# Kernel optimization log

Measured on AMD Instinct MI355X. Metric: run time of the kernel, lower is better.

The kernel has to match this reference:

```python
import jax, jax.numpy as jnp
import numpy as np

C = 256  # input_channels == output_channels (residual add requires it)
EPS = 1e-5


def conv1d(x, w, b):
    # x: [B, Cin, L], w: [Cout, Cin, K], 'same' padding for K=3,p=1
    y = jax.lax.conv_general_dilated(x, w, window_strides=(1,), padding=[(1, 1)],
                                     dimension_numbers=('NCH', 'OIH', 'NCH'))
    return y + b[None, :, None]


def batchnorm(x, gamma, beta):
    # training-mode BN over (batch, length) per channel, biased variance
    m = jnp.mean(x, axis=(0, 2), keepdims=True)
    v = jnp.var(x, axis=(0, 2), keepdims=True)
    return (x - m) * jax.lax.rsqrt(v + EPS) * gamma[None, :, None] + beta[None, :, None]


def cross_attn(q_in, kv_in, res, qw, qb, kw, kb, vw, vb, ow, ob, g, be):
    q = conv1d(q_in, qw, qb)   # [B, C, L]
    k = conv1d(kv_in, kw, kb)  # [B, C, L]
    v = conv1d(kv_in, vw, vb)  # [B, C, L]
    scores = jnp.einsum('bcl,bcm->blm', q, k) / jnp.sqrt(jnp.float32(C))
    probs = jax.nn.softmax(scores, axis=-1)          # [B, L, L]
    ctx = jnp.einsum('blm,bcm->bcl', probs, v)       # [B, C, L]
    return batchnorm(conv1d(ctx, ow, ob), g, be) + res


def setup_inputs() -> dict:
    key = jax.random.key(0)
    ks = jax.random.split(key, 24)
    B, L = 16, 1024
    d = {
        'image': jax.random.normal(ks[0], (B, C, L), jnp.float32),
        'clinical': jax.random.normal(ks[1], (B, 1, L), jnp.float32),
    }
    def w(k, shape):
        return jax.random.normal(k, shape, jnp.float32) * 0.05
    # branch a: cli_to_img (query from image, key/value from clinical)
    d['a_qw'] = w(ks[2], (C, C, 3)); d['a_qb'] = w(ks[3], (C,))
    d['a_kw'] = w(ks[4], (C, 1, 3)); d['a_kb'] = w(ks[5], (C,))
    d['a_vw'] = w(ks[6], (C, 1, 3)); d['a_vb'] = w(ks[7], (C,))
    d['a_ow'] = w(ks[8], (C, C, 3)); d['a_ob'] = w(ks[9], (C,))
    d['a_g'] = jnp.ones((C,), jnp.float32); d['a_beta'] = jnp.zeros((C,), jnp.float32)
    # branch b: img_to_cli (query from clinical, key/value from image)
    d['b_qw'] = w(ks[10], (C, 1, 3)); d['b_qb'] = w(ks[11], (C,))
    d['b_kw'] = w(ks[12], (C, C, 3)); d['b_kb'] = w(ks[13], (C,))
    d['b_vw'] = w(ks[14], (C, C, 3)); d['b_vb'] = w(ks[15], (C,))
    d['b_ow'] = w(ks[16], (C, C, 3)); d['b_ob'] = w(ks[17], (C,))
    d['b_g'] = jnp.ones((C,), jnp.float32); d['b_beta'] = jnp.zeros((C,), jnp.float32)
    return d


def reference(image, clinical,
              a_qw, a_qb, a_kw, a_kb, a_vw, a_vb, a_ow, a_ob, a_g, a_beta,
              b_qw, b_qb, b_kw, b_kb, b_vw, b_vb, b_ow, b_ob, b_g, b_beta):
    cli_to_img = cross_attn(image, clinical, image,
                            a_qw, a_qb, a_kw, a_kb, a_vw, a_vb, a_ow, a_ob, a_g, a_beta)
    img_to_cli = cross_attn(clinical, image, image,
                            b_qw, b_qb, b_kw, b_kb, b_vw, b_vb, b_ow, b_ob, b_g, b_beta)
    return jnp.concatenate([cli_to_img, img_to_cli], axis=1)  # [B, 2C, L]
```

## Files before the change

kernel.cpp:

```cpp
#include <hip/hip_runtime.h>


typedef short bf16x8 __attribute__((ext_vector_type(8)));
typedef float f32x4 __attribute__((ext_vector_type(4)));

__device__ __forceinline__ unsigned short f2bf(float f) {
    union { float f; unsigned u; } v; v.f = f;
    unsigned r = v.u + 0x7fffu + ((v.u >> 16) & 1u);
    return (unsigned short)(r >> 16);
}
__device__ __forceinline__ float bf2f(unsigned short h) {
    union { unsigned u; float f; } v; v.u = ((unsigned)h) << 16;
    return v.f;
}

__device__ __forceinline__ void glds16(const void* g, void* l) {
    __builtin_amdgcn_global_load_lds(
        (const __attribute__((address_space(1))) unsigned int*)g,
        (__attribute__((address_space(3))) unsigned int*)l, 16, 0, 0);
}

#define TM 128
#define TN 128
#define BK 32

struct GOp {
    const unsigned short* A; const unsigned short* B; void* C;
    long sA, sB, sC;
    int lda, ldb, ldc, nxt, nyt;
    const float* bias_row; const float* bias_col;
};

template<bool OUT_BF16>
__global__ __launch_bounds__(256)
void gemm_nt(GOp op0, GOp op1, int n0, int K, float alpha)
{
    __shared__ __attribute__((aligned(16))) char sh[34816];
    unsigned short* shs = (unsigned short*)sh;
    int id = blockIdx.x;
    const bool brn = (id >= n0);
    const GOp op = brn ? op1 : op0;
    if (brn) id -= n0;
    const int perz = op.nxt * op.nyt;
    const int bz = id / perz;
    const int rem = id - bz * perz;
    const int by = rem / op.nxt;
    const int bx = rem - by * op.nxt;

    const unsigned short* Ab = op.A + op.sA * bz;
    const unsigned short* Bb = op.B + op.sB * bz;
    const int lda = op.lda, ldb = op.ldb;
    const int i0 = by * TM;
    const int j0 = bx * TN;
    const int t = threadIdx.x;
    const int lane = t & 63;
    const int wave = t >> 6;
    const int wm = wave & 1, wn = wave >> 1;

    const int srow = wave * 16 + (lane >> 2);
    const int sc8 = (lane & 3) * 8;
    const unsigned short* gA0 = Ab + (long)(i0 + srow) * lda + sc8;
    const unsigned short* gA1 = gA0 + (long)64 * lda;
    const unsigned short* gB0 = Bb + (long)(j0 + srow) * ldb + sc8;
    const unsigned short* gB1 = gB0 + (long)64 * ldb;
    const int d0 = wave * 512;
    const int d1 = 2048 + wave * 512;

    f32x4 acc[4][4];
#pragma unroll
    for (int a_ = 0; a_ < 4; ++a_)
#pragma unroll
        for (int b_ = 0; b_ < 4; ++b_)
            acc[a_][b_] = (f32x4){0.f, 0.f, 0.f, 0.f};

    const int frow = lane & 15;
    const int fk = (lane >> 4) * 8;

    glds16(gA0, shs + d0);
    glds16(gA1, shs + d1);
    glds16(gB0, shs + 8192 + d0);
    glds16(gB1, shs + 8192 + d1);

    int cur = 0;
    for (int k0 = 0; k0 < K; k0 += BK) {
        __syncthreads();
        const int kn = k0 + BK;
        if (kn < K) {
            const int nb = cur ^ 1;
            glds16(gA0 + kn, shs + nb * 4096 + d0);
            glds16(gA1 + kn, shs + nb * 4096 + d1);
            glds16(gB0 + kn, shs + 8192 + nb * 4096 + d0);
            glds16(gB1 + kn, shs + 8192 + nb * 4096 + d1);
        }
        const unsigned short* la = shs + cur * 4096;
        const unsigned short* lb = shs + 8192 + cur * 4096;
        bf16x8 af[4], bfr[4];
#pragma unroll
        for (int mt = 0; mt < 4; ++mt)
            af[mt] = *(const bf16x8*)(&la[(wm * 64 + mt * 16 + frow) * BK + fk]);
#pragma unroll
        for (int nt = 0; nt < 4; ++nt)
            bfr[nt] = *(const bf16x8*)(&lb[(wn * 64 + nt * 16 + frow) * BK + fk]);
#pragma unroll
        for (int mt = 0; mt < 4; ++mt)
#pragma unroll
            for (int nt = 0; nt < 4; ++nt)
                acc[mt][nt] = __builtin_amdgcn_mfma_f32_16x16x32_bf16(af[mt], bfr[nt], acc[mt][nt], 0, 0, 0);
        cur ^= 1;
    }

    const int lr = (lane >> 4) * 4;
    const int lc = lane & 15;
    __syncthreads();

    if (OUT_BF16) {
        unsigned short* tile = shs;
#pragma unroll
        for (int mt = 0; mt < 4; ++mt) {
#pragma unroll
            for (int nt = 0; nt < 4; ++nt) {
                const int col = wn * 64 + nt * 16 + lc;
                const float bc = op.bias_col ? op.bias_col[j0 + col] : 0.f;
#pragma unroll
                for (int r = 0; r < 4; ++r) {
                    const int row = wm * 64 + mt * 16 + lr + r;
                    const float brv = op.bias_row ? op.bias_row[i0 + row] : 0.f;
                    tile[row * 136 + col] = f2bf(acc[mt][nt][r] * alpha + brv + bc);
                }
            }
        }
        __syncthreads();
        unsigned short* Cb = (unsigned short*)op.C + op.sC * bz;
#pragma unroll
        for (int p = 0; p < 8; ++p) {
            const int cid = p * 256 + t;
            const int row = cid >> 4;
            const int c8 = (cid & 15) * 8;
            const uint4 v = *(const uint4*)(tile + row * 136 + c8);
            *(uint4*)(Cb + (long)(i0 + row) * op.ldc + j0 + c8) = v;
        }
    } else {
        float* tileF = (float*)sh;
        float* Cb = (float*)op.C + op.sC * bz;
#pragma unroll
        for (int h = 0; h < 2; ++h) {
            if (wm == h) {
#pragma unroll
                for (int mt = 0; mt < 4; ++mt) {
#pragma unroll
                    for (int nt = 0; nt < 4; ++nt) {
                        const int col = wn * 64 + nt * 16 + lc;
                        const float bc = op.bias_col ? op.bias_col[j0 + col] : 0.f;
#pragma unroll
                        for (int r = 0; r < 4; ++r) {
                            const int rl = mt * 16 + lr + r;
                            const float brv = op.bias_row ? op.bias_row[i0 + h * 64 + rl] : 0.f;
                            tileF[rl * 132 + col] = acc[mt][nt][r] * alpha + brv + bc;
                        }
                    }
                }
            }
            __syncthreads();
#pragma unroll
            for (int p = 0; p < 8; ++p) {
                const int cid = p * 256 + t;
                const int rl = cid >> 5;
                const int c4 = (cid & 31) * 4;
                const float4 v = *(const float4*)(tileF + rl * 132 + c4);
                *(float4*)(Cb + (long)(i0 + h * 64 + rl) * op.ldc + j0 + c4) = v;
            }
            __syncthreads();
        }
    }
}

__global__ __launch_bounds__(256)
void flash_attn(const unsigned short* __restrict__ QK,
                const unsigned short* __restrict__ qTb,
                const unsigned short* __restrict__ kTa,
                const unsigned short* __restrict__ va,
                const unsigned short* __restrict__ vb,
                unsigned short* __restrict__ ctxT)
{
    __shared__ __attribute__((aligned(16))) char sh[53248];
    unsigned short* Qs = (unsigned short*)sh;
    unsigned short* Ps = (unsigned short*)(sh + 33792);
    float* lts = (float*)(sh + 51200);

    const long sQK = 1024L * 512, sQT = 1024L * 256, sV = 256L * 1024;
    const int bid = blockIdx.x;
    const int z = bid >> 4;
    const int l0 = (bid & 15) * 64;
    const bool bb = (z >= 16);
    const int zz = bb ? z - 16 : z;
    const unsigned short* Qg = bb ? (qTb + (long)zz * sQT) : (QK + (long)zz * sQK);
    const int ldq = bb ? 256 : 512;
    const unsigned short* Kg = bb ? (QK + (long)zz * sQK + 256) : (kTa + (long)zz * sQT);
    const int ldk = bb ? 512 : 256;
    const unsigned short* Vg = (bb ? vb : va) + (long)zz * sV;
    unsigned short* Og = ctxT + ((long)z * 1026 + 1 + l0) * 256;
    const unsigned short* Qb = Qg + (long)l0 * ldq;

    const int t = threadIdx.x;
    const int lane = t & 63, w = t >> 6;
    const int g = lane >> 4, li = lane & 15;

#pragma unroll
    for (int p = 0; p < 8; ++p) {
        const int cid = p * 256 + t, row = cid >> 5, c8 = (cid & 31) * 8;
        const uint4 v = *(const uint4*)(Qb + (long)row * ldq + c8);
        *(uint4*)(Qs + row * 264 + c8) = v;
    }
    __syncthreads();

    f32x4 acc_o[4][4];
    f32x4 l_run[4];
#pragma unroll
    for (int mt = 0; mt < 4; ++mt) {
        l_run[mt] = (f32x4){0.f, 0.f, 0.f, 0.f};
#pragma unroll
        for (int nt = 0; nt < 4; ++nt)
            acc_o[mt][nt] = (f32x4){0.f, 0.f, 0.f, 0.f};
    }

    for (int m0 = 0; m0 < 1024; m0 += 128) {
        f32x4 acc_s[4][2];
#pragma unroll
        for (int mt = 0; mt < 4; ++mt) {
            acc_s[mt][0] = (f32x4){0.f, 0.f, 0.f, 0.f};
            acc_s[mt][1] = (f32x4){0.f, 0.f, 0.f, 0.f};
        }
        const unsigned short* Kt = Kg + (long)(m0 + w * 32) * ldk;
#pragma unroll
        for (int kt = 0; kt < 8; ++kt) {
            const bf16x8 bk0 = *(const bf16x8*)(Kt + (long)li * ldk + kt * 32 + g * 8);
            const bf16x8 bk1 = *(const bf16x8*)(Kt + (long)(16 + li) * ldk + kt * 32 + g * 8);
#pragma unroll
            for (int mt = 0; mt < 4; ++mt) {
                const bf16x8 aq = *(const bf16x8*)(Qs + (mt * 16 + li) * 264 + kt * 32 + g * 8);
                acc_s[mt][0] = __builtin_amdgcn_mfma_f32_16x16x32_bf16(aq, bk0, acc_s[mt][0], 0, 0, 0);
                acc_s[mt][1] = __builtin_amdgcn_mfma_f32_16x16x32_bf16(aq, bk1, acc_s[mt][1], 0, 0, 0);
            }
        }
        f32x4 rs[4];
#pragma unroll
        for (int mt = 0; mt < 4; ++mt) {
            rs[mt] = (f32x4){0.f, 0.f, 0.f, 0.f};
#pragma unroll
            for (int nt = 0; nt < 2; ++nt)
#pragma unroll
                for (int r = 0; r < 4; ++r) {
                    const float pv = __expf(acc_s[mt][nt][r] * 0.0625f);
                    acc_s[mt][nt][r] = pv;
                    rs[mt][r] += pv;
                }
        }
#pragma unroll
        for (int mask = 1; mask <= 8; mask <<= 1)
#pragma unroll
            for (int mt = 0; mt < 4; ++mt)
#pragma unroll
                for (int r = 0; r < 4; ++r)
                    rs[mt][r] += __shfl_xor(rs[mt][r], mask);
#pragma unroll
        for (int mt = 0; mt < 4; ++mt)
#pragma unroll
            for (int nt = 0; nt < 2; ++nt)
#pragma unroll
                for (int r = 0; r < 4; ++r)
                    Ps[(mt * 16 + g * 4 + r) * 136 + w * 32 + nt * 16 + li] =
                        f2bf(acc_s[mt][nt][r]);
        if (li == 0)
#pragma unroll
            for (int mt = 0; mt < 4; ++mt)
                *(f32x4*)(lts + w * 64 + mt * 16 + g * 4) = rs[mt];
        __syncthreads();
#pragma unroll
        for (int mt = 0; mt < 4; ++mt) {
            const int off = mt * 16 + g * 4;
            const f32x4 s0 = *(const f32x4*)(lts + off);
            const f32x4 s1 = *(const f32x4*)(lts + 64 + off);
            const f32x4 s2 = *(const f32x4*)(lts + 128 + off);
            const f32x4 s3 = *(const f32x4*)(lts + 192 + off);
            l_run[mt] += s0 + s1 + s2 + s3;
        }
#pragma unroll
        for (int kt2 = 0; kt2 < 4; ++kt2) {
            bf16x8 bv[4];
#pragma unroll
            for (int nt2 = 0; nt2 < 4; ++nt2)
                bv[nt2] = *(const bf16x8*)(Vg + (long)(w * 64 + nt2 * 16 + li) * 1024
                                           + m0 + kt2 * 32 + g * 8);
#pragma unroll
            for (int mt = 0; mt < 4; ++mt) {
                const bf16x8 ap = *(const bf16x8*)(Ps + (mt * 16 + li) * 136 + kt2 * 32 + g * 8);
#pragma unroll
                for (int nt2 = 0; nt2 < 4; ++nt2)
                    acc_o[mt][nt2] = __builtin_amdgcn_mfma_f32_16x16x32_bf16(ap, bv[nt2], acc_o[mt][nt2], 0, 0, 0);
            }
        }
        __syncthreads();
    }

    f32x4 inv[4];
#pragma unroll
    for (int mt = 0; mt < 4; ++mt)
#pragma unroll
        for (int r = 0; r < 4; ++r)
            inv[mt][r] = 1.f / l_run[mt][r];
#pragma unroll
    for (int mt = 0; mt < 4; ++mt)
#pragma unroll
        for (int nt2 = 0; nt2 < 4; ++nt2)
#pragma unroll
            for (int r = 0; r < 4; ++r)
                Qs[(mt * 16 + g * 4 + r) * 264 + w * 64 + nt2 * 16 + li] =
                    f2bf(acc_o[mt][nt2][r] * inv[mt][r]);
    __syncthreads();
#pragma unroll
    for (int p = 0; p < 8; ++p) {
        const int cid = p * 256 + t, row = cid >> 5, c8 = (cid & 31) * 8;
        *(uint4*)(Og + (long)row * 256 + c8) = *(const uint4*)(Qs + row * 264 + c8);
    }
}

__global__ __launch_bounds__(256)
void prep(const float* __restrict__ image, const float* __restrict__ cli,
          const float* __restrict__ a_qw, const float* __restrict__ a_qb,
          const float* __restrict__ a_kw, const float* __restrict__ a_kb,
          const float* __restrict__ a_vw, const float* __restrict__ a_vb,
          const float* __restrict__ a_ow,
          const float* __restrict__ b_qw, const float* __restrict__ b_qb,
          const float* __restrict__ b_kw, const float* __restrict__ b_kb,
          const float* __restrict__ b_vw, const float* __restrict__ b_vb,
          const float* __restrict__ b_ow,
          unsigned short* __restrict__ imgT, unsigned short* __restrict__ ctxT,
          unsigned short* __restrict__ kTa, unsigned short* __restrict__ va,
          unsigned short* __restrict__ qTb,
          unsigned short* __restrict__ W, float* __restrict__ qkb)
{
    __shared__ char smem[64 * 65 * 4];
    const int b = blockIdx.x;
    const int t = threadIdx.x;
    if (b < 1024) {
        float* tile = (float*)smem;
        const int bt = b >> 6, rem = b & 63;
        const int l0 = (rem & 15) * 64, c0 = (rem >> 4) * 64;
        const float* xb = image + ((long)bt * 256 + c0) * 1024 + l0;
        for (int idx = t; idx < 4096; idx += 256) {
            const int cc = idx >> 6, ll = idx & 63;
            tile[cc * 65 + ll] = xb[(long)cc * 1024 + ll];
        }
        __syncthreads();
        unsigned short* op = imgT + ((long)bt * 1026 + l0 + 1) * 256 + c0;
        for (int idx = t; idx < 4096; idx += 256) {
            const int ll = idx >> 6, cc = idx & 63;
            op[(long)ll * 256 + cc] = f2bf(tile[cc * 65 + ll]);
        }
    } else if (b < 1536) {
        float* xs = (float*)smem;
        const int local = b - 1024;
        const int bz = local >> 5;
        const int l0 = (local & 31) * 32;
        if (t < 34) {
            const int l = l0 + t - 1;
            xs[t] = (l >= 0 && l < 1024) ? cli[(long)bz * 1024 + l] : 0.f;
        }
        __syncthreads();
        for (int i = t; i < 32 * 256; i += 256) {
            const int r = i >> 8, c = i & 255;
            const float x0 = xs[r], x1 = xs[r + 1], x2 = xs[r + 2];
            const float kv = a_kw[c * 3] * x0 + a_kw[c * 3 + 1] * x1 + a_kw[c * 3 + 2] * x2 + a_kb[c];
            const float qv = b_qw[c * 3] * x0 + b_qw[c * 3 + 1] * x1 + b_qw[c * 3 + 2] * x2 + b_qb[c];
            const long base = ((long)bz * 1024 + l0 + r) * 256 + c;
            kTa[base] = f2bf(kv);
            qTb[base] = f2bf(qv);
        }
        for (int i = t; i < 32 * 256; i += 256) {
            const int c = i >> 5, r = i & 31;
            const float x0 = xs[r], x1 = xs[r + 1], x2 = xs[r + 2];
            const float vv = a_vw[c * 3] * x0 + a_vw[c * 3 + 1] * x1 + a_vw[c * 3 + 2] * x2 + a_vb[c];
            va[((long)bz * 256 + c) * 1024 + l0 + r] = f2bf(vv);
        }
    } else if (b < 5376) {
        const int i = (b - 1536) * 256 + t;
        const int row = i / 768;
        const int kk = i - row * 768;
        const int j = kk >> 8, ci = kk & 255;
        const float* src = (row < 256) ? a_qw : (row < 512) ? b_kw
                         : (row < 768) ? b_vw : (row < 1024) ? a_ow : b_ow;
        const int r = row & 255;
        W[i] = f2bf(src[r * 768 + ci * 3 + j]);
    } else {
        const int i = (b - 5376) * 256 + t;
        if (i < 512) {
            qkb[i] = (i < 256) ? a_qb[i] : b_kb[i - 256];
        } else if (i < 512 + 8192) {
            const int p = i - 512;
            const int bi = p >> 9, rr = (p >> 8) & 1, c = p & 255;
            imgT[((long)bi * 1026 + (rr ? 1025 : 0)) * 256 + c] = 0;
        } else {
            const int p = i - 512 - 8192;
            const int bz = p >> 9, rr = (p >> 8) & 1, c = p & 255;
            ctxT[((long)bz * 1026 + (rr ? 1025 : 0)) * 256 + c] = 0;
        }
    }
}

__global__ __launch_bounds__(256)
void bn_stats(const float* __restrict__ Y,
              const float* __restrict__ ag, const float* __restrict__ abeta,
              const float* __restrict__ bg, const float* __restrict__ bbeta,
              float* __restrict__ ss)
{
    const int ch = blockIdx.x;
    const int branch = ch >> 8, c = ch & 255;
    const int t = threadIdx.x;
    float s = 0.f, s2 = 0.f;
    for (int idx = t; idx < 16 * 1024; idx += 256) {
        const int b = idx >> 10, l = idx & 1023;
        const float v = Y[(((long)(branch * 16 + b)) * 256 + c) * 1024 + l];
        s += v; s2 += v * v;
    }
#pragma unroll
    for (int off = 32; off; off >>= 1) { s += __shfl_xor(s, off); s2 += __shfl_xor(s2, off); }
    __shared__ float r1[4], r2[4];
    const int wave = t >> 6, lane = t & 63;
    if (lane == 0) { r1[wave] = s; r2[wave] = s2; }
    __syncthreads();
    if (t == 0) {
        s = r1[0] + r1[1] + r1[2] + r1[3];
        s2 = r2[0] + r2[1] + r2[2] + r2[3];
        const float mean = s * (1.f / 16384.f);
        const float var = s2 * (1.f / 16384.f) - mean * mean;
        const float inv = rsqrtf(var + 1e-5f);
        const float g = branch ? bg[c] : ag[c];
        const float be = branch ? bbeta[c] : abeta[c];
        const float sc = g * inv;
        ss[ch] = sc;
        ss[512 + ch] = be - mean * sc;
    }
}

__global__ __launch_bounds__(256)
void bn_apply(const float* __restrict__ Y, const float* __restrict__ img,
              const float* __restrict__ ss, float* __restrict__ out)
{
    const long i4 = (long)blockIdx.x * 256 + threadIdx.x;
    const long e = i4 * 4;
    const int l = (int)(e & 1023);
    const int ch = (int)((e >> 10) & 511);
    const int b = (int)(e >> 19);
    const int branch = ch >> 8, c = ch & 255;
    const float sc = ss[ch], sh = ss[512 + ch];
    const long yoff = (((long)(branch * 16 + b)) * 256 + c) * 1024 + l;
    const long ioff = ((long)b * 256 + c) * 1024 + l;
    const float4 yv = *(const float4*)(Y + yoff);
    const float4 iv = *(const float4*)(img + ioff);
    float4 o;
    o.x = yv.x * sc + sh + iv.x;
    o.y = yv.y * sc + sh + iv.y;
    o.z = yv.z * sc + sh + iv.z;
    o.w = yv.w * sc + sh + iv.w;
    *(float4*)(out + e) = o;
}

extern "C" void kernel_launch(void* const* d_in, const int* in_sizes, int n_in,
                              void* d_out, int out_size, void* d_ws, size_t ws_size,
                              hipStream_t stream)
{
    const float* image    = (const float*)d_in[0];
    const float* clinical = (const float*)d_in[1];
    const float* a_qw = (const float*)d_in[2];  const float* a_qb = (const float*)d_in[3];
    const float* a_kw = (const float*)d_in[4];  const float* a_kb = (const float*)d_in[5];
    const float* a_vw = (const float*)d_in[6];  const float* a_vb = (const float*)d_in[7];
    const float* a_ow = (const float*)d_in[8];  const float* a_ob = (const float*)d_in[9];
    const float* a_g  = (const float*)d_in[10]; const float* a_be = (const float*)d_in[11];
    const float* b_qw = (const float*)d_in[12]; const float* b_qb = (const float*)d_in[13];
    const float* b_kw = (const float*)d_in[14]; const float* b_kb = (const float*)d_in[15];
    const float* b_vw = (const float*)d_in[16]; const float* b_vb = (const float*)d_in[17];
    const float* b_ow = (const float*)d_in[18]; const float* b_ob = (const float*)d_in[19];
    const float* b_g  = (const float*)d_in[20]; const float* b_be = (const float*)d_in[21];
    float* out = (float*)d_out;

    char* ws = (char*)d_ws;
    const long MB = 1048576L;
    unsigned short* imgT = (unsigned short*)(ws);
    unsigned short* ctxT = (unsigned short*)(ws + 9 * MB);
    unsigned short* kTa  = (unsigned short*)(ws + 27 * MB);
    unsigned short* qTb  = (unsigned short*)(ws + 36 * MB);
    unsigned short* va   = (unsigned short*)(ws + 46 * MB);
    unsigned short* vb   = (unsigned short*)(ws + 54 * MB);
    unsigned short* QK   = (unsigned short*)(ws + 62 * MB);
    float*          Y    = (float*)(ws + 142 * MB);
    unsigned short* W    = (unsigned short*)(ws + 174 * MB);
    float*          qkb  = (float*)(ws + 176 * MB);
    float*          ss   = qkb + 512;
    unsigned short* Wqk = W;
    unsigned short* Wvb = W + 512L * 768;
    unsigned short* Woa = W + 768L * 768;
    unsigned short* Wob = W + 1024L * 768;

    const dim3 blk(256);
    const long sIT = 1026L * 256, sQK = 1024L * 512,
               sV = 256L * 1024;

    prep<<<5474, blk, 0, stream>>>(image, clinical,
                                   a_qw, a_qb, a_kw, a_kb, a_vw, a_vb, a_ow,
                                   b_qw, b_qb, b_kw, b_kb, b_vw, b_vb, b_ow,
                                   imgT, ctxT, kTa, va, qTb, W, qkb);
    {
        GOp opQ = {imgT, Wqk, QK, sIT, 0, sQK, 256, 768, 512, 4, 8, nullptr, qkb};
        GOp opV = {Wvb, imgT, vb, 0, sIT, sV, 768, 256, 1024, 8, 2, b_vb, nullptr};
        gemm_nt<true><<<768, blk, 0, stream>>>(opQ, opV, 512, 768, 1.f);
    }
    flash_attn<<<512, blk, 0, stream>>>(QK, qTb, kTa, va, vb, ctxT);
    {
        GOp opA = {Woa, ctxT, Y, 0, sIT, sV, 768, 256, 1024, 8, 2, a_ob, nullptr};
        GOp opB = {Wob, ctxT + 16 * sIT, Y + 16 * sV, 0, sIT, sV, 768, 256, 1024, 8, 2, b_ob, nullptr};
        gemm_nt<false><<<512, blk, 0, stream>>>(opA, opB, 256, 768, 1.f);
    }
    bn_stats<<<512, blk, 0, stream>>>(Y, a_g, a_be, b_g, b_be, ss);
    bn_apply<<<8192, blk, 0, stream>>>(Y, image, ss, out);
}
```

Baseline: 296.9 us.

## Fuse BN statistics into output GEMM epilogue and store conv output as bf16

The output-projection GEMM now writes its result in bf16 rather than fp32. Per-channel sum and sum-of-squares are accumulated in the GEMM epilogue with atomics, so the separate BN statistics pass over Y becomes a tiny finalize kernel. The block index order in the GEMM and attention kernels is changed so that batch varies fastest, which may improve cache reuse of shared weights. This halves Y traffic and removes a full reread, at the cost of bf16 rounding of pre-BN activations and nondeterministic atomic summation.

```diff
diff --git a/kernel.cpp b/kernel.cpp
--- a/kernel.cpp
+++ b/kernel.cpp
@@ -27,11 +27,11 @@
 struct GOp {
     const unsigned short* A; const unsigned short* B; void* C;
     long sA, sB, sC;
-    int lda, ldb, ldc, nxt, nyt;
+    int lda, ldb, ldc, nxt, nyt, nz;
     const float* bias_row; const float* bias_col;
+    float* stats; int stat_base;
 };
 
-template<bool OUT_BF16>
 __global__ __launch_bounds__(256)
 void gemm_nt(GOp op0, GOp op1, int n0, int K, float alpha)
 {
@@ -41,9 +41,8 @@
     const bool brn = (id >= n0);
     const GOp op = brn ? op1 : op0;
     if (brn) id -= n0;
-    const int perz = op.nxt * op.nyt;
-    const int bz = id / perz;
-    const int rem = id - bz * perz;
+    const int bz = id % op.nz;
+    const int rem = id / op.nz;
     const int by = rem / op.nxt;
     const int bx = rem - by * op.nxt;
 
@@ -113,63 +112,49 @@
     const int lc = lane & 15;
     __syncthreads();
 
-    if (OUT_BF16) {
-        unsigned short* tile = shs;
-#pragma unroll
-        for (int mt = 0; mt < 4; ++mt) {
-#pragma unroll
-            for (int nt = 0; nt < 4; ++nt) {
-                const int col = wn * 64 + nt * 16 + lc;
-                const float bc = op.bias_col ? op.bias_col[j0 + col] : 0.f;
-#pragma unroll
-                for (int r = 0; r < 4; ++r) {
-                    const int row = wm * 64 + mt * 16 + lr + r;
-                    const float brv = op.bias_row ? op.bias_row[i0 + row] : 0.f;
-                    tile[row * 136 + col] = f2bf(acc[mt][nt][r] * alpha + brv + bc);
-                }
+    unsigned short* tile = shs;
+#pragma unroll
+    for (int mt = 0; mt < 4; ++mt) {
+#pragma unroll
+        for (int nt = 0; nt < 4; ++nt) {
+            const int col = wn * 64 + nt * 16 + lc;
+            const float bc = op.bias_col ? op.bias_col[j0 + col] : 0.f;
+#pragma unroll
+            for (int r = 0; r < 4; ++r) {
+                const int row = wm * 64 + mt * 16 + lr + r;
+                const float brv = op.bias_row ? op.bias_row[i0 + row] : 0.f;
+                tile[row * 136 + col] = f2bf(acc[mt][nt][r] * alpha + brv + bc);
             }
         }
-        __syncthreads();
-        unsigned short* Cb = (unsigned short*)op.C + op.sC * bz;
-#pragma unroll
-        for (int p = 0; p < 8; ++p) {
-            const int cid = p * 256 + t;
-            const int row = cid >> 4;
-            const int c8 = (cid & 15) * 8;
-            const uint4 v = *(const uint4*)(tile + row * 136 + c8);
-            *(uint4*)(Cb + (long)(i0 + row) * op.ldc + j0 + c8) = v;
-        }
-    } else {
-        float* tileF = (float*)sh;
-        float* Cb = (float*)op.C + op.sC * bz;
-#pragma unroll
-        for (int h = 0; h < 2; ++h) {
-            if (wm == h) {
-#pragma unroll
-                for (int mt = 0; mt < 4; ++mt) {
-#pragma unroll
-                    for (int nt = 0; nt < 4; ++nt) {
-                        const int col = wn * 64 + nt * 16 + lc;
-                        const float bc = op.bias_col ? op.bias_col[j0 + col] : 0.f;
-#pragma unroll
-                        for (int r = 0; r < 4; ++r) {
-                            const int rl = mt * 16 + lr + r;
-                            const float brv = op.bias_row ? op.bias_row[i0 + h * 64 + rl] : 0.f;
-                            tileF[rl * 132 + col] = acc[mt][nt][r] * alpha + brv + bc;
-                        }
-                    }
-                }
+    }
+    __syncthreads();
+    unsigned short* Cb = (unsigned short*)op.C + op.sC * bz;
+#pragma unroll
+    for (int p = 0; p < 8; ++p) {
+        const int cid = p * 256 + t;
+        const int row = cid >> 4;
+        const int c8 = (cid & 15) * 8;
+        const uint4 v = *(const uint4*)(tile + row * 136 + c8);
+        *(uint4*)(Cb + (long)(i0 + row) * op.ldc + j0 + c8) = v;
+    }
+    if (op.stats) {
+        const int row = t >> 1, half = t & 1;
+        float s = 0.f, s2 = 0.f;
+#pragma unroll
+        for (int c = 0; c < 64; c += 8) {
+            const bf16x8 v = *(const bf16x8*)(tile + row * 136 + half * 64 + c);
+#pragma unroll
+            for (int e = 0; e < 8; ++e) {
+                const float f = bf2f((unsigned short)v[e]);
+                s += f; s2 += f * f;
             }
-            __syncthreads();
-#pragma unroll
-            for (int p = 0; p < 8; ++p) {
-                const int cid = p * 256 + t;
-                const int rl = cid >> 5;
-                const int c4 = (cid & 31) * 4;
-                const float4 v = *(const float4*)(tileF + rl * 132 + c4);
-                *(float4*)(Cb + (long)(i0 + h * 64 + rl) * op.ldc + j0 + c4) = v;
-            }
-            __syncthreads();
+        }
+        s += __shfl_xor(s, 1);
+        s2 += __shfl_xor(s2, 1);
+        if (half == 0) {
+            const int ch = op.stat_base + i0 + row;
+            atomicAdd(&op.stats[ch], s);
+            atomicAdd(&op.stats[512 + ch], s2);
         }
     }
 }
@@ -189,8 +174,8 @@
 
     const long sQK = 1024L * 512, sQT = 1024L * 256, sV = 256L * 1024;
     const int bid = blockIdx.x;
-    const int z = bid >> 4;
-    const int l0 = (bid & 15) * 64;
+    const int z = bid & 31;
+    const int l0 = (bid >> 5) * 64;
     const bool bb = (z >= 16);
     const int zz = bb ? z - 16 : z;
     const unsigned short* Qg = bb ? (qTb + (long)zz * sQT) : (QK + (long)zz * sQK);
@@ -337,7 +322,8 @@
           unsigned short* __restrict__ imgT, unsigned short* __restrict__ ctxT,
           unsigned short* __restrict__ kTa, unsigned short* __restrict__ va,
           unsigned short* __restrict__ qTb,
-          unsigned short* __restrict__ W, float* __restrict__ qkb)
+          unsigned short* __restrict__ W, float* __restrict__ qkb,
+          float* __restrict__ sums)
 {
     __shared__ char smem[64 * 65 * 4];
     const int b = blockIdx.x;
@@ -399,51 +385,36 @@
             const int p = i - 512;
             const int bi = p >> 9, rr = (p >> 8) & 1, c = p & 255;
             imgT[((long)bi * 1026 + (rr ? 1025 : 0)) * 256 + c] = 0;
-        } else {
+        } else if (i < 512 + 8192 + 16384) {
             const int p = i - 512 - 8192;
             const int bz = p >> 9, rr = (p >> 8) & 1, c = p & 255;
             ctxT[((long)bz * 1026 + (rr ? 1025 : 0)) * 256 + c] = 0;
+        } else if (i < 512 + 8192 + 16384 + 1024) {
+            sums[i - 512 - 8192 - 16384] = 0.f;
         }
     }
 }
 
 __global__ __launch_bounds__(256)
-void bn_stats(const float* __restrict__ Y,
-              const float* __restrict__ ag, const float* __restrict__ abeta,
-              const float* __restrict__ bg, const float* __restrict__ bbeta,
-              float* __restrict__ ss)
-{
-    const int ch = blockIdx.x;
+void bn_finalize(const float* __restrict__ sums,
+                 const float* __restrict__ ag, const float* __restrict__ abeta,
+                 const float* __restrict__ bg, const float* __restrict__ bbeta,
+                 float* __restrict__ ss)
+{
+    const int ch = blockIdx.x * 256 + threadIdx.x;
     const int branch = ch >> 8, c = ch & 255;
-    const int t = threadIdx.x;
-    float s = 0.f, s2 = 0.f;
-    for (int idx = t; idx < 16 * 1024; idx += 256) {
-        const int b = idx >> 10, l = idx & 1023;
-        const float v = Y[(((long)(branch * 16 + b)) * 256 + c) * 1024 + l];
-        s += v; s2 += v * v;
-    }
-#pragma unroll
-    for (int off = 32; off; off >>= 1) { s += __shfl_xor(s, off); s2 += __shfl_xor(s2, off); }
-    __shared__ float r1[4], r2[4];
-    const int wave = t >> 6, lane = t & 63;
-    if (lane == 0) { r1[wave] = s; r2[wave] = s2; }
-    __syncthreads();
-    if (t == 0) {
-        s = r1[0] + r1[1] + r1[2] + r1[3];
-        s2 = r2[0] + r2[1] + r2[2] + r2[3];
-        const float mean = s * (1.f / 16384.f);
-        const float var = s2 * (1.f / 16384.f) - mean * mean;
-        const float inv = rsqrtf(var + 1e-5f);
-        const float g = branch ? bg[c] : ag[c];
-        const float be = branch ? bbeta[c] : abeta[c];
-        const float sc = g * inv;
-        ss[ch] = sc;
-        ss[512 + ch] = be - mean * sc;
-    }
+    const float mean = sums[ch] * (1.f / 16384.f);
+    const float var = sums[512 + ch] * (1.f / 16384.f) - mean * mean;
+    const float inv = rsqrtf(var + 1e-5f);
+    const float g = branch ? bg[c] : ag[c];
+    const float be = branch ? bbeta[c] : abeta[c];
+    const float sc = g * inv;
+    ss[ch] = sc;
+    ss[512 + ch] = be - mean * sc;
 }
 
 __global__ __launch_bounds__(256)
-void bn_apply(const float* __restrict__ Y, const float* __restrict__ img,
+void bn_apply(const unsigned short* __restrict__ Y, const float* __restrict__ img,
               const float* __restrict__ ss, float* __restrict__ out)
 {
     const long i4 = (long)blockIdx.x * 256 + threadIdx.x;
@@ -455,13 +426,13 @@
     const float sc = ss[ch], sh = ss[512 + ch];
     const long yoff = (((long)(branch * 16 + b)) * 256 + c) * 1024 + l;
     const long ioff = ((long)b * 256 + c) * 1024 + l;
-    const float4 yv = *(const float4*)(Y + yoff);
+    const ushort4 yv = *(const ushort4*)(Y + yoff);
     const float4 iv = *(const float4*)(img + ioff);
     float4 o;
-    o.x = yv.x * sc + sh + iv.x;
-    o.y = yv.y * sc + sh + iv.y;
-    o.z = yv.z * sc + sh + iv.z;
-    o.w = yv.w * sc + sh + iv.w;
+    o.x = bf2f(yv.x) * sc + sh + iv.x;
+    o.y = bf2f(yv.y) * sc + sh + iv.y;
+    o.z = bf2f(yv.z) * sc + sh + iv.z;
+    o.w = bf2f(yv.w) * sc + sh + iv.w;
     *(float4*)(out + e) = o;
 }
 
@@ -492,34 +463,34 @@
     unsigned short* va   = (unsigned short*)(ws + 46 * MB);
     unsigned short* vb   = (unsigned short*)(ws + 54 * MB);
     unsigned short* QK   = (unsigned short*)(ws + 62 * MB);
-    float*          Y    = (float*)(ws + 142 * MB);
+    unsigned short* Y    = (unsigned short*)(ws + 142 * MB);
     unsigned short* W    = (unsigned short*)(ws + 174 * MB);
     float*          qkb  = (float*)(ws + 176 * MB);
     float*          ss   = qkb + 512;
+    float*          sums = qkb + 1536;
     unsigned short* Wqk = W;
     unsigned short* Wvb = W + 512L * 768;
     unsigned short* Woa = W + 768L * 768;
     unsigned short* Wob = W + 1024L * 768;
 
     const dim3 blk(256);
-    const long sIT = 1026L * 256, sQK = 1024L * 512,
-               sV = 256L * 1024;
-
-    prep<<<5474, blk, 0, stream>>>(image, clinical,
+    const long sIT = 1026L * 256, sQK = 1024L * 512, sV = 256L * 1024;
+
+    prep<<<5478, blk, 0, stream>>>(image, clinical,
                                    a_qw, a_qb, a_kw, a_kb, a_vw, a_vb, a_ow,
                                    b_qw, b_qb, b_kw, b_kb, b_vw, b_vb, b_ow,
-                                   imgT, ctxT, kTa, va, qTb, W, qkb);
+                                   imgT, ctxT, kTa, va, qTb, W, qkb, sums);
     {
-        GOp opQ = {imgT, Wqk, QK, sIT, 0, sQK, 256, 768, 512, 4, 8, nullptr, qkb};
-        GOp opV = {Wvb, imgT, vb, 0, sIT, sV, 768, 256, 1024, 8, 2, b_vb, nullptr};
-        gemm_nt<true><<<768, blk, 0, stream>>>(opQ, opV, 512, 768, 1.f);
+        GOp opQ = {imgT, Wqk, QK, sIT, 0, sQK, 256, 768, 512, 4, 8, 16, nullptr, qkb, nullptr, 0};
+        GOp opV = {Wvb, imgT, vb, 0, sIT, sV, 768, 256, 1024, 8, 2, 16, b_vb, nullptr, nullptr, 0};
+        gemm_nt<<<768, blk, 0, stream>>>(opQ, opV, 512, 768, 1.f);
     }
     flash_attn<<<512, blk, 0, stream>>>(QK, qTb, kTa, va, vb, ctxT);
     {
-        GOp opA = {Woa, ctxT, Y, 0, sIT, sV, 768, 256, 1024, 8, 2, a_ob, nullptr};
-        GOp opB = {Wob, ctxT + 16 * sIT, Y + 16 * sV, 0, sIT, sV, 768, 256, 1024, 8, 2, b_ob, nullptr};
-        gemm_nt<false><<<512, blk, 0, stream>>>(opA, opB, 256, 768, 1.f);
-    }
-    bn_stats<<<512, blk, 0, stream>>>(Y, a_g, a_be, b_g, b_be, ss);
+        GOp opA = {Woa, ctxT, Y, 0, sIT, sV, 768, 256, 1024, 8, 2, 16, a_ob, nullptr, sums, 0};
+        GOp opB = {Wob, ctxT + 16 * sIT, Y + 16 * sV, 0, sIT, sV, 768, 256, 1024, 8, 2, 16, b_ob, nullptr, sums, 256};
+        gemm_nt<<<512, blk, 0, stream>>>(opA, opB, 256, 768, 1.f);
+    }
+    bn_finalize<<<2, blk, 0, stream>>>(sums, a_g, a_be, b_g, b_be, ss);
     bn_apply<<<8192, blk, 0, stream>>>(Y, image, ss, out);
 }
```

Measured after the change: 267.9 us. 9.8% less time.
